# Performance work log

Hardware: AMD Instinct MI355X
Metric: run time of the kernel (lower is better)

Reference implementation:

```python
import jax, jax.numpy as jnp
import numpy as np

B = 262144
D = 128          # d_model
DFF = 4 * D      # 512, FFN expansion
T = 16           # num_tiles
TPC = 4          # tiles_per_cluster
NC = T // TPC    # 4 clusters
NOPS = 8         # len(OPCODES)
EMB = 32
FEAT = EMB + 17  # 49
TW, SW, DW = 0.01, 0.005, 0.01  # ternary / sparsity / diversity weights


def ternary_quant(W):
    # per-tile ternary quantization: threshold at 0.7 * mean|W|, scale = mean|W|
    s0 = jnp.mean(jnp.abs(W))
    return s0 * jnp.sign(W) * (jnp.abs(W) > 0.7 * s0).astype(W.dtype)


def setup_inputs() -> dict:
    key = jax.random.key(0)
    ks = jax.random.split(key, 16)
    inp = {
        'op_idx': jax.random.randint(ks[0], (B,), 0, NOPS),
        'a': jax.random.randint(ks[1], (B,), 0, 256),
        'b': jax.random.randint(ks[2], (B,), 0, 256),
        'c': jax.random.randint(ks[3], (B,), 0, 2),
        # parameters
        'op_embed': jax.random.normal(ks[4], (NOPS, EMB), jnp.float32),
        'W_in': jax.random.normal(ks[5], (FEAT, D), jnp.float32) / np.sqrt(FEAT),
        'b_in': jnp.zeros((D,), jnp.float32),
        'Wr': jax.random.normal(ks[6], (D, T), jnp.float32) / np.sqrt(D),
        'W1': jax.random.normal(ks[7], (T, D, DFF), jnp.float32) / np.sqrt(D),
        'W2': jax.random.normal(ks[8], (T, DFF, D), jnp.float32) / np.sqrt(DFF),
        'Wh1': jax.random.normal(ks[9], (D, 64), jnp.float32) / np.sqrt(D),
        'bh1': jnp.zeros((64,), jnp.float32),
        'Wh2': jax.random.normal(ks[10], (64, 8), jnp.float32) / np.sqrt(64),
        'bh2': jnp.zeros((8,), jnp.float32),
    }
    return inp


def reference(op_embed, W_in, b_in, Wr, W1, W2, Wh1, bh1, Wh2, bh2, op_idx, a, b, c):
    bits = lambda v: ((v[:, None] >> jnp.arange(8)) & 1).astype(jnp.float32)  # [B,8]
    emb = op_embed[op_idx]  # [B,32]
    x = jnp.concatenate([emb, bits(a), bits(b), c[:, None].astype(jnp.float32)], axis=1)  # [B,49]
    x = x @ W_in + b_in  # [B,D]

    # tile routing (top-1)
    logits = x @ Wr                      # [B,T]
    probs = jax.nn.softmax(logits, -1)
    idx = jnp.argmax(probs, -1)          # [B]
    gate = jnp.max(probs, -1)            # [B]

    # ternary-quantized per-tile FFN weights
    W1q = jax.vmap(ternary_quant)(W1)    # [T,D,DFF]
    W2q = jax.vmap(ternary_quant)(W2)    # [T,DFF,D]

    out = jnp.zeros_like(x)
    for t in range(T):  # fixed small tile set
        y = jax.nn.gelu(x @ W1q[t]) @ W2q[t]          # [B,D]
        out = out + jnp.where((idx == t)[:, None], y, 0.0)
    out = out * gate[:, None]

    # aux losses
    one_hot = jax.nn.one_hot(idx, T, dtype=x.dtype)
    frac = one_hot.mean(0)               # tokens per tile
    meanp = probs.mean(0)                # mean router prob per tile
    sparsity = T * jnp.sum(frac * meanp)              # load-balance (Switch-style)
    tern = jnp.mean(jnp.abs(W1 - W1q)) + jnp.mean(jnp.abs(W2 - W2q))
    cp = meanp.reshape(NC, TPC).sum(-1)               # cluster usage
    diversity = jnp.sum(cp * jnp.log(cp + 1e-9))      # negative entropy
    aux = TW * tern + SW * sparsity + DW * diversity

    h = jax.nn.relu(out @ Wh1 + bh1)
    result = jax.nn.sigmoid(h @ Wh2 + bh2)  # [B,8]
    return result, idx, aux
```

## Files before the change

kernel.cpp:

```cpp
#include <hip/hip_runtime.h>
#include <hip/hip_bf16.h>
#include <math.h>

typedef __attribute__((ext_vector_type(8))) short short8;
typedef __attribute__((ext_vector_type(4))) float floatx4;
typedef __attribute__((ext_vector_type(4))) unsigned int uintx4;

__device__ __forceinline__ unsigned short f2bf(float f) {
    unsigned int u = __float_as_uint(f);
    unsigned int r = (u + 0x7fffu + ((u >> 16) & 1u)) >> 16;
    return (unsigned short)r;
}

__device__ __forceinline__ unsigned int cvtpk(float a, float b) {
    unsigned int r;
    asm("v_cvt_pk_bf16_f32 %0, %1, %2" : "=v"(r) : "v"(a), "v"(b));
    return r;
}

__device__ __forceinline__ void permlane32_swap(unsigned int &a, unsigned int &b) {
    asm volatile("v_permlane32_swap_b32 %0, %1" : "+v"(a), "+v"(b));
}
__device__ __forceinline__ void permlane16_swap(unsigned int &a, unsigned int &b) {
    asm volatile("v_permlane16_swap_b32 %0, %1" : "+v"(a), "+v"(b));
}

__device__ __forceinline__ float gelu_f(float u) {
    float u2 = u * u;
    float p = __builtin_fmaf(u2, -0.102943242f, -2.302208184f);
    float z = p * u;
    float e;
    asm("v_exp_f32 %0, %1" : "=v"(e) : "v"(z));
    return u * __builtin_amdgcn_rcpf(1.0f + e);
}

__device__ __forceinline__ floatx4 mfma16(short8 a, short8 b, floatx4 c) {
    return __builtin_amdgcn_mfma_f32_16x16x32_bf16(a, b, c, 0, 0, 0);
}


__global__ __launch_bounds__(256) void k_prep1(
        const float* __restrict__ W1, const float* __restrict__ W2,
        float* __restrict__ partials,
        const float* __restrict__ op_embed, const float* __restrict__ W_in,
        const float* __restrict__ b_in,
        float* embW, float* Ta, float* Tb, float* Tc) {
    __shared__ float red[256];
    int bid = blockIdx.x;
    if (bid < 512) {
        bool isW1 = bid < 256;
        const float* W = (isW1 ? W1 : W2) + (long)(isW1 ? bid : bid - 256) * 4096;
        float s = 0.f;
        #pragma unroll
        for (int i = 0; i < 4; i++) {
            floatx4 v = *(const floatx4*)(W + i * 1024 + threadIdx.x * 4);
            s += fabsf(v[0]) + fabsf(v[1]) + fabsf(v[2]) + fabsf(v[3]);
        }
        red[threadIdx.x] = s; __syncthreads();
        for (int st = 128; st > 0; st >>= 1) {
            if (threadIdx.x < st) red[threadIdx.x] += red[threadIdx.x + st];
            __syncthreads();
        }
        if (threadIdx.x == 0) partials[bid] = red[0];
    } else {
        int i = (bid - 512) * 256 + threadIdx.x;
        if (i < 1024) {
            int op = i >> 7, j = i & 127;
            float s = b_in[j];
            #pragma unroll
            for (int k = 0; k < 32; k++) s += op_embed[op * 32 + k] * W_in[k * 128 + j];
            embW[i] = s;
        } else if (i < 1024 + 32768) {
            int r = i - 1024; int a = r >> 7, j = r & 127;
            float s = 0.f;
            #pragma unroll
            for (int bit = 0; bit < 8; bit++) if ((a >> bit) & 1) s += W_in[(32 + bit) * 128 + j];
            Ta[r] = s;
        } else if (i < 33792 + 32768) {
            int r = i - 33792; int b = r >> 7, j = r & 127;
            float s = 0.f;
            #pragma unroll
            for (int bit = 0; bit < 8; bit++) if ((b >> bit) & 1) s += W_in[(40 + bit) * 128 + j];
            Tb[r] = s;
        } else if (i < 66560 + 128) {
            int j = i - 66560; Tc[j] = W_in[48 * 128 + j];
        }
    }
}


__global__ __launch_bounds__(256) void k_prep2(
        const float* __restrict__ W1, const float* __restrict__ W2,
        const float* __restrict__ partials,
        unsigned short* __restrict__ W1qT, unsigned short* __restrict__ W2qT,
        float* ternsum,
        const float* __restrict__ embW, const float* __restrict__ Ta,
        const float* __restrict__ Tb, const float* __restrict__ Tc,
        const float* __restrict__ Wr,
        float* embWr, float* TaR, float* TbR, float* TcR) {
    __shared__ unsigned short Lq[4096];
    __shared__ float red[256];
    int blk = blockIdx.x;
    if (blk >= 512) {
        int i = (blk - 512) * 256 + threadIdx.x;
        int row = i >> 4, t = i & 15;
        const float* src; float* dst;
        if (row < 8)        { src = embW + row * 128;        dst = embWr + i; }
        else if (row < 264) { src = Ta + (row - 8) * 128;    dst = TaR + (row - 8) * 16 + t; }
        else if (row < 520) { src = Tb + (row - 264) * 128;  dst = TbR + (row - 264) * 16 + t; }
        else if (row == 520){ src = Tc;                      dst = TcR + t; }
        else return;
        float s = 0.f;
        for (int j = 0; j < 128; j++) s += src[j] * Wr[j * 16 + t];
        *dst = s;
        return;
    }
    bool isW1 = blk < 256;
    int rb = isW1 ? blk : blk - 256;
    int t = rb >> 4, slab = rb & 15;
    const float* part = partials + (isW1 ? 0 : 256) + t * 16;
    float ssum = 0.f;
    #pragma unroll
    for (int i = 0; i < 16; i++) ssum += part[i];
    float s = ssum * (1.0f / 65536.0f);
    float thr = 0.7f * s;
    unsigned int us = (unsigned int)f2bf(s);
    int tid = threadIdx.x;
    float dsum = 0.f;
    if (isW1) {
        int f0 = slab * 32;
        int d = tid >> 1, fh = (tid & 1) * 16;
        const float* src = W1 + (long)t * 65536 + d * 512 + f0 + fh;
        #pragma unroll
        for (int i = 0; i < 4; i++) {
            floatx4 w = *(const floatx4*)(src + i * 4);
            #pragma unroll
            for (int r = 0; r < 4; r++) {
                float wv = w[r];
                float aw = fabsf(wv);
                bool big = aw > thr;
                dsum += big ? fabsf(aw - s) : aw;
                unsigned int sign15 = (__float_as_uint(wv) >> 16) & 0x8000u;
                unsigned short q = big ? (unsigned short)(us | sign15) : (unsigned short)0;
                Lq[(fh + i * 4 + r) * 128 + d] = q;
            }
        }
    } else {
        int d0 = slab * 8;
        int f = tid * 2;
        const float* src = W2 + (long)t * 65536 + f * 128 + d0;
        #pragma unroll
        for (int rr = 0; rr < 2; rr++) {
            #pragma unroll
            for (int i = 0; i < 2; i++) {
                floatx4 w = *(const floatx4*)(src + rr * 128 + i * 4);
                #pragma unroll
                for (int r = 0; r < 4; r++) {
                    float wv = w[r];
                    float aw = fabsf(wv);
                    bool big = aw > thr;
                    dsum += big ? fabsf(aw - s) : aw;
                    unsigned int sign15 = (__float_as_uint(wv) >> 16) & 0x8000u;
                    unsigned short q = big ? (unsigned short)(us | sign15) : (unsigned short)0;
                    Lq[(i * 4 + r) * 512 + f + rr] = q;
                }
            }
        }
    }
    __syncthreads();
    unsigned short* dst = (isW1 ? W1qT : W2qT) + (long)t * 65536 + slab * 4096;
    const uintx4* Ls = (const uintx4*)Lq;
    uintx4* D4 = (uintx4*)dst;
    D4[tid] = Ls[tid];
    D4[tid + 256] = Ls[tid + 256];
    red[tid] = dsum; __syncthreads();
    for (int st2 = 128; st2 > 0; st2 >>= 1) {
        if (tid < st2) red[tid] += red[tid + st2];
        __syncthreads();
    }
    if (tid == 0) atomicAdd(ternsum, red[0]);
}


__global__ __launch_bounds__(256) void k_main3(
        const int* __restrict__ op_idx, const int* __restrict__ a_in,
        const int* __restrict__ b_in_i, const int* __restrict__ c_in,
        const float* __restrict__ embWr, const float* __restrict__ TaR,
        const float* __restrict__ TbR, const float* __restrict__ TcR,
        float* __restrict__ gate_out,
        float* psum, int* cnt, float* __restrict__ d_idx,
        const unsigned short* __restrict__ W2qT, const float* __restrict__ Wh1,
        unsigned short* __restrict__ W23qT) {
    __shared__ float sp[4][16];
    __shared__ int sc[4][16];
    __shared__ float wcol[128];

    if (blockIdx.x >= 1024) {
        int b2 = blockIdx.x - 1024;
        int t = b2 >> 6, h = b2 & 63;
        if (threadIdx.x < 128) wcol[threadIdx.x] = Wh1[threadIdx.x * 64 + h];
        __syncthreads();
        int k2 = threadIdx.x * 2;
        const unsigned short* w2 = W2qT + (long)t * 65536 + k2;
        float a0 = 0.f, a1 = 0.f;
        #pragma unroll 8
        for (int d = 0; d < 128; d++) {
            unsigned int u = *(const unsigned int*)(w2 + d * 512);
            float w = wcol[d];
            a0 += w * __uint_as_float(u << 16);
            a1 += w * __uint_as_float(u & 0xffff0000u);
        }
        *(unsigned int*)(W23qT + ((long)(t * 64 + h)) * 512 + k2) = cvtpk(a0, a1);
        return;
    }

    int gid = blockIdx.x * 256 + threadIdx.x;
    int lane = threadIdx.x & 63;
    int j = lane & 15;
    int grpbase = lane & 48;
    float psum_acc = 0.f; int cnt_acc = 0;

    #pragma unroll 1
    for (int it = 0; it < 16; it++) {
        int tok = it * 16384 + (gid >> 4);
        int op = op_idx[tok], a = a_in[tok], b = b_in_i[tok], c = c_in[tok];
        float cf = (float)c;

        float lg = embWr[op * 16 + j] + TaR[a * 16 + j] + TbR[b * 16 + j] + cf * TcR[j];
        float m = lg;
        m = fmaxf(m, __shfl_xor(m, 8, 16));
        m = fmaxf(m, __shfl_xor(m, 4, 16));
        m = fmaxf(m, __shfl_xor(m, 2, 16));
        m = fmaxf(m, __shfl_xor(m, 1, 16));
        float p = __expf(lg - m);
        float s = p;
        s += __shfl_xor(s, 8, 16);
        s += __shfl_xor(s, 4, 16);
        s += __shfl_xor(s, 2, 16);
        s += __shfl_xor(s, 1, 16);
        float g = __builtin_amdgcn_rcpf(s);
        unsigned long long ball = __ballot(lg == m);
        int bi = __ffsll((unsigned long long)((ball >> grpbase) & 0xffffULL)) - 1;
        psum_acc += p * g;
        cnt_acc += (j == bi) ? 1 : 0;
        if (j == 0) { gate_out[tok] = g; d_idx[tok] = (float)bi; }
    }

    psum_acc += __shfl_xor(psum_acc, 16);
    psum_acc += __shfl_xor(psum_acc, 32);
    cnt_acc += __shfl_xor(cnt_acc, 16);
    cnt_acc += __shfl_xor(cnt_acc, 32);
    int wv = threadIdx.x >> 6;
    if (lane < 16) { sp[wv][j] = psum_acc; sc[wv][j] = cnt_acc; }
    __syncthreads();
    if (threadIdx.x < 16) {
        int jj = threadIdx.x;
        atomicAdd(&psum[jj], sp[0][jj] + sp[1][jj] + sp[2][jj] + sp[3][jj]);
        atomicAdd(&cnt[jj], sc[0][jj] + sc[1][jj] + sc[2][jj] + sc[3][jj]);
    }
}


__global__ void k_scatter(const float* __restrict__ d_idx, const int* __restrict__ cnt,
                          int* fill, int* __restrict__ bucket) {
    __shared__ int lc[16], lbase[16];
    if (threadIdx.x < 16) lc[threadIdx.x] = 0;
    __syncthreads();
    int offs[16];
    {
        int off = 0;
        #pragma unroll
        for (int tt = 0; tt < 16; tt++) { offs[tt] = off; off += cnt[tt]; }
    }
    int tok = blockIdx.x * 256 + threadIdx.x;
    int t = (int)d_idx[tok];
    int lpos = atomicAdd(&lc[t], 1);
    __syncthreads();
    if (threadIdx.x < 16) lbase[threadIdx.x] = atomicAdd(&fill[threadIdx.x], lc[threadIdx.x]);
    __syncthreads();
    bucket[offs[t] + lbase[t] + lpos] = tok;
}


__global__ __launch_bounds__(256, 3) void k_ffn(
    const int* __restrict__ op_idx, const int* __restrict__ a_in,
    const int* __restrict__ b_in_i, const int* __restrict__ c_in,
    const float* __restrict__ embW, const float* __restrict__ Ta,
    const float* __restrict__ Tb, const float* __restrict__ Tc,
    const float* __restrict__ gate,
    const int* __restrict__ bucket, const int* __restrict__ cnt_g,
    const float* __restrict__ psum_g, const float* __restrict__ ternsum_g,
    const unsigned short* __restrict__ W1qT, const unsigned short* __restrict__ W23qT,
    const float* __restrict__ Wh2, const float* __restrict__ bh1,
    const float* __restrict__ bh2,
    float* __restrict__ result, float* __restrict__ d_aux) {

    extern __shared__ __align__(16) unsigned char smem[];
    unsigned short* Ax = (unsigned short*)smem;
    float* Red = (float*)(smem + 17408);
    int*   toks = (int*)(smem + 33792);
    float* gats = (float*)(smem + 34048);
    float* Wh2l = (float*)(smem + 34304);
    float* bh2l = (float*)(smem + 36352);
    float* bh1l = (float*)(smem + 36384);
    int*   opsl = (int*)(smem + 36640);
    int*   asl  = (int*)(smem + 36896);
    int*   bsl  = (int*)(smem + 37152);
    float* csl  = (float*)(smem + 37408);

    int bid = blockIdx.x;
    int t = -1, ci = 0, nt = 0, base = 0;
    {
        int coff = 0, off = 0;
        #pragma unroll 1
        for (int tt = 0; tt < 16; tt++) {
            int c = cnt_g[tt];
            int ch = (c + 63) >> 6;
            if (t < 0 && bid < coff + ch) { t = tt; ci = bid - coff; nt = c; base = off + ci * 64; }
            coff += ch; off += c;
        }
    }
    if (t < 0) return;
    int nvalid = nt - ci * 64; if (nvalid > 64) nvalid = 64;

    int tid = threadIdx.x;
    if (tid < 64) {
        int tk = (tid < nvalid) ? bucket[base + tid] : -1;
        toks[tid] = tk;
        int tks = (tk >= 0) ? tk : 0;
        gats[tid] = (tk >= 0) ? gate[tk] : 0.0f;
        opsl[tid] = op_idx[tks];
        asl[tid]  = a_in[tks];
        bsl[tid]  = b_in_i[tks];
        csl[tid]  = (float)c_in[tks];
    }
    Wh2l[tid] = Wh2[tid];
    Wh2l[tid + 256] = Wh2[tid + 256];
    if (tid < 8) bh2l[tid] = bh2[tid];
    else if (tid < 72) bh1l[tid - 8] = bh1[tid - 8];
    __syncthreads();

    #pragma unroll
    for (int it = 0; it < 4; it++) {
        int seg = it * 256 + tid; int r = seg >> 4, sg = seg & 15;
        int d0 = sg * 8;
        int op = opsl[r], a = asl[r], b = bsl[r];
        float cf = csl[r];
        const floatx4* Ev = (const floatx4*)(embW + op * 128 + d0);
        const floatx4* A4 = (const floatx4*)(Ta + a * 128 + d0);
        const floatx4* B4 = (const floatx4*)(Tb + b * 128 + d0);
        const floatx4* C4 = (const floatx4*)(Tc + d0);
        floatx4 v0 = Ev[0] + A4[0] + B4[0] + cf * C4[0];
        floatx4 v1 = Ev[1] + A4[1] + B4[1] + cf * C4[1];
        uintx4 o;
        o[0] = cvtpk(v0[0], v0[1]);
        o[1] = cvtpk(v0[2], v0[3]);
        o[2] = cvtpk(v1[0], v1[1]);
        o[3] = cvtpk(v1[2], v1[3]);
        *(uintx4*)(Ax + r * 136 + sg * 8) = o;
    }
    __syncthreads();

    int lane = tid & 63, dh = tid >> 6;
    int lane15 = lane & 15, lgrp = lane >> 4;

    floatx4 acc3[4][4];
    #pragma unroll
    for (int i = 0; i < 4; i++)
        #pragma unroll
        for (int j = 0; j < 4; j++) acc3[i][j] = (floatx4){0.f, 0.f, 0.f, 0.f};

    const unsigned short* w1p  = W1qT + (long)t * 65536 + (dh * 32 + lane15) * 128 + lgrp * 8;
    const unsigned short* w23p = W23qT + (long)t * 32768 + lane15 * 512 + dh * 32 + lgrp * 8;
    int ho0 = dh * 8192;
    int ho1 = ((dh + 1) & 3) * 8192;
    int ho2 = ((dh + 2) & 3) * 8192;
    int ho3 = ((dh + 3) & 3) * 8192;

    #pragma unroll
    for (int nc = 0; nc < 4; nc++) {
        const unsigned short* w1c = w1p + nc * 16384;
        const unsigned short* w23c = w23p + nc * 128;

        short8 a00 = *(const short8*)(w1c + 0 * 32);
        short8 a01 = *(const short8*)(w1c + 1 * 32);
        short8 a02 = *(const short8*)(w1c + 2 * 32);
        short8 a03 = *(const short8*)(w1c + 3 * 32);
        short8 a10 = *(const short8*)(w1c + 2048 + 0 * 32);
        short8 a11 = *(const short8*)(w1c + 2048 + 1 * 32);
        short8 a12 = *(const short8*)(w1c + 2048 + 2 * 32);
        short8 a13 = *(const short8*)(w1c + 2048 + 3 * 32);
        short8 af23_0 = *(const short8*)(w23c + ho0);
        short8 af23_1 = *(const short8*)(w23c + ho1);
        short8 af23_2 = *(const short8*)(w23c + ho2);
        short8 af23_3 = *(const short8*)(w23c + ho3);

        floatx4 acc1[2][4];
        #pragma unroll
        for (int i = 0; i < 2; i++)
            #pragma unroll
            for (int j = 0; j < 4; j++) acc1[i][j] = (floatx4){0.f, 0.f, 0.f, 0.f};

        #pragma unroll
        for (int mt = 0; mt < 4; mt++) {
            int mrow = (mt * 16 + lane15) * 136;
            short8 bf0 = *(const short8*)(Ax + mrow + 0 * 32 + lgrp * 8);
            short8 bf1 = *(const short8*)(Ax + mrow + 1 * 32 + lgrp * 8);
            short8 bf2 = *(const short8*)(Ax + mrow + 2 * 32 + lgrp * 8);
            short8 bf3 = *(const short8*)(Ax + mrow + 3 * 32 + lgrp * 8);
            acc1[0][mt] = mfma16(a00, bf0, acc1[0][mt]);
            acc1[1][mt] = mfma16(a10, bf0, acc1[1][mt]);
            acc1[0][mt] = mfma16(a01, bf1, acc1[0][mt]);
            acc1[1][mt] = mfma16(a11, bf1, acc1[1][mt]);
            acc1[0][mt] = mfma16(a02, bf2, acc1[0][mt]);
            acc1[1][mt] = mfma16(a12, bf2, acc1[1][mt]);
            acc1[0][mt] = mfma16(a03, bf3, acc1[0][mt]);
            acc1[1][mt] = mfma16(a13, bf3, acc1[1][mt]);
        }

        #pragma unroll
        for (int mt = 0; mt < 4; mt++) {
            floatx4 v0 = acc1[0][mt], v1 = acc1[1][mt];
            unsigned int X0 = cvtpk(gelu_f(v0[0]), gelu_f(v0[1]));
            unsigned int X1 = cvtpk(gelu_f(v0[2]), gelu_f(v0[3]));
            unsigned int Y0 = cvtpk(gelu_f(v1[0]), gelu_f(v1[1]));
            unsigned int Y1 = cvtpk(gelu_f(v1[2]), gelu_f(v1[3]));
            permlane32_swap(X0, Y0);
            permlane16_swap(X0, Y0);
            permlane32_swap(X1, Y1);
            permlane16_swap(X1, Y1);
            union { uintx4 u; short8 s; } bu;
            bu.u[0] = X0; bu.u[1] = X1; bu.u[2] = Y0; bu.u[3] = Y1;
            short8 bfrag = bu.s;
            acc3[0][mt] = mfma16(af23_0, bfrag, acc3[0][mt]);
            acc3[1][mt] = mfma16(af23_1, bfrag, acc3[1][mt]);
            acc3[2][mt] = mfma16(af23_2, bfrag, acc3[2][mt]);
            acc3[3][mt] = mfma16(af23_3, bfrag, acc3[3][mt]);
        }
    }

    floatx4 fin[4];
    #pragma unroll
    for (int mt = 0; mt < 4; mt++) fin[mt] = acc3[0][mt];
    float* myslot = Red + dh * 1024;
    int lofs = lane * 4;
    #pragma unroll
    for (int mt = 0; mt < 4; mt++)
        *(floatx4*)(myslot + mt * 256 + lofs) = acc3[1][mt];
    __syncthreads();
    {
        const float* ps = Red + ((dh + 3) & 3) * 1024;
        #pragma unroll
        for (int mt = 0; mt < 4; mt++)
            fin[mt] += *(const floatx4*)(ps + mt * 256 + lofs);
    }
    __syncthreads();
    #pragma unroll
    for (int mt = 0; mt < 4; mt++)
        *(floatx4*)(myslot + mt * 256 + lofs) = acc3[2][mt];
    __syncthreads();
    {
        const float* ps = Red + ((dh + 2) & 3) * 1024;
        #pragma unroll
        for (int mt = 0; mt < 4; mt++)
            fin[mt] += *(const floatx4*)(ps + mt * 256 + lofs);
    }
    __syncthreads();
    #pragma unroll
    for (int mt = 0; mt < 4; mt++)
        *(floatx4*)(myslot + mt * 256 + lofs) = acc3[3][mt];
    __syncthreads();
    {
        const float* ps = Red + ((dh + 1) & 3) * 1024;
        #pragma unroll
        for (int mt = 0; mt < 4; mt++)
            fin[mt] += *(const floatx4*)(ps + mt * 256 + lofs);
    }

    float* H = (float*)Ax;
    int hb = dh * 16 + lgrp * 4;
    floatx4 b4 = *(const floatx4*)(bh1l + hb);
    #pragma unroll
    for (int mt = 0; mt < 4; mt++) {
        int m = mt * 16 + lane15;
        float gm = gats[m];
        floatx4 v;
        v[0] = fmaxf(fin[mt][0] * gm + b4[0], 0.f);
        v[1] = fmaxf(fin[mt][1] * gm + b4[1], 0.f);
        v[2] = fmaxf(fin[mt][2] * gm + b4[2], 0.f);
        v[3] = fmaxf(fin[mt][3] * gm + b4[3], 0.f);
        *(floatx4*)(H + m * 68 + hb) = v;
    }
    __syncthreads();

    int mloc = tid >> 2, c0 = (tid & 3) * 2;
    int tk = toks[mloc];
    float z0 = bh2l[c0], z1 = bh2l[c0 + 1];
    const floatx4* Hr4 = (const floatx4*)(H + mloc * 68);
    #pragma unroll
    for (int h4 = 0; h4 < 16; h4++) {
        floatx4 hv = Hr4[h4];
        #pragma unroll
        for (int r = 0; r < 4; r++) {
            int h = h4 * 4 + r;
            z0 += hv[r] * Wh2l[h * 8 + c0];
            z1 += hv[r] * Wh2l[h * 8 + c0 + 1];
        }
    }
    if (tk >= 0) {
        float2 rr;
        rr.x = __builtin_amdgcn_rcpf(1.0f + __expf(-z0));
        rr.y = __builtin_amdgcn_rcpf(1.0f + __expf(-z1));
        *(float2*)(result + (long)tk * 8 + c0) = rr;
    }

    if (bid == 0 && tid == 0) {
        const float Bf = 262144.0f;
        float tern = ternsum_g[0] * (1.0f / 1048576.0f);
        float sp = 0.f; float cp[4] = {0.f, 0.f, 0.f, 0.f};
        for (int tt = 0; tt < 16; tt++) {
            float frac = (float)cnt_g[tt] / Bf, mp = psum_g[tt] / Bf;
            sp += frac * mp; cp[tt >> 2] += mp;
        }
        float dv = 0.f;
        for (int cc = 0; cc < 4; cc++) dv += cp[cc] * logf(cp[cc] + 1e-9f);
        d_aux[0] = 0.01f * tern + 0.005f * (16.0f * sp) + 0.01f * dv;
    }
}


extern "C" void kernel_launch(void* const* d_in, const int* in_sizes, int n_in,
                              void* d_out, int out_size, void* d_ws, size_t ws_size,
                              hipStream_t stream) {
    const int* op_idx = (const int*)d_in[0];
    const int* a_in   = (const int*)d_in[1];
    const int* b_in_i = (const int*)d_in[2];
    const int* c_in   = (const int*)d_in[3];
    const float* op_embed = (const float*)d_in[4];
    const float* W_in  = (const float*)d_in[5];
    const float* b_in  = (const float*)d_in[6];
    const float* Wr    = (const float*)d_in[7];
    const float* W1    = (const float*)d_in[8];
    const float* W2    = (const float*)d_in[9];
    const float* Wh1   = (const float*)d_in[10];
    const float* bh1   = (const float*)d_in[11];
    const float* Wh2   = (const float*)d_in[12];
    const float* bh2   = (const float*)d_in[13];

    const long B = in_sizes[0];
    float* result = (float*)d_out;
    float* d_idx  = (float*)d_out + B * 8;
    float* d_aux  = (float*)d_out + B * 9;

    unsigned char* ws = (unsigned char*)d_ws;
    unsigned short* W1qT  = (unsigned short*)(ws + 67108864);
    unsigned short* W2qT  = (unsigned short*)(ws + 69206016);
    unsigned short* W23qT = (unsigned short*)(ws + 71303168);
    float* gate  = (float*)(ws + 72351744);
    int*   bucket= (int*)  (ws + 73400320);
    float* Ta    = (float*)(ws + 74448896);
    float* Tb    = (float*)(ws + 74579968);
    float* embW  = (float*)(ws + 74711040);
    float* Tc    = (float*)(ws + 74715136);
    float* TaR   = (float*)(ws + 74715648);
    float* TbR   = (float*)(ws + 74732032);
    float* embWr = (float*)(ws + 74748416);
    float* TcR   = (float*)(ws + 74748928);
    float* partials = (float*)(ws + 74748992);
    unsigned char* acc = ws + 74751040;
    float* ternsum = (float*)(acc + 0);
    float* psum    = (float*)(acc + 64);
    int*   cnt     = (int*)(acc + 128);
    int*   fill    = (int*)(acc + 192);

    hipMemsetAsync(acc, 0, 256, stream);

    k_prep1<<<773, 256, 0, stream>>>(W1, W2, partials, op_embed, W_in, b_in,
                                     embW, Ta, Tb, Tc);
    k_prep2<<<545, 256, 0, stream>>>(W1, W2, partials, W1qT, W2qT, ternsum,
                                     embW, Ta, Tb, Tc, Wr, embWr, TaR, TbR, TcR);
    k_main3<<<2048, 256, 0, stream>>>(op_idx, a_in, b_in_i, c_in,
                                      embWr, TaR, TbR, TcR,
                                      gate, psum, cnt, d_idx,
                                      W2qT, Wh1, W23qT);
    k_scatter<<<(int)(B / 256), 256, 0, stream>>>(d_idx, cnt, fill, bucket);
    k_ffn<<<4112, 256, 37664, stream>>>(op_idx, a_in, b_in_i, c_in,
                                        embW, Ta, Tb, Tc,
                                        gate, bucket, cnt, psum, ternsum,
                                        W1qT, W23qT, Wh2, bh1, bh2, result, d_aux);
}
```

Baseline: 264.4 us.

## Fuse token scatter into router kernel using fixed-capacity per-tile buckets

Removes the separate k_scatter launch by having the router kernel record each token's tile and block-local position in shared memory, then reserve a global slice with one atomic per tile and write bucket entries directly. Buckets become fixed-capacity per-tile regions (BUCKET_CAP), so no prefix sum over counts is needed and the FFN kernel indexes tile*CAP. The FFN first GEMM is also restructured into a kk loop that loads W1 fragments per step instead of holding all eight at once, which lowers register pressure. The costs are a larger bucket workspace and extra shared atomics inside the router loop.

```diff
diff --git a/kernel.cpp b/kernel.cpp
--- a/kernel.cpp
+++ b/kernel.cpp
@@ -5,6 +5,8 @@
 typedef __attribute__((ext_vector_type(8))) short short8;
 typedef __attribute__((ext_vector_type(4))) float floatx4;
 typedef __attribute__((ext_vector_type(4))) unsigned int uintx4;
+
+#define BUCKET_CAP 262144
 
 __device__ __forceinline__ unsigned short f2bf(float f) {
     unsigned int u = __float_as_uint(f);
@@ -188,12 +190,16 @@
         const float* __restrict__ embWr, const float* __restrict__ TaR,
         const float* __restrict__ TbR, const float* __restrict__ TcR,
         float* __restrict__ gate_out,
-        float* psum, int* cnt, float* __restrict__ d_idx,
+        float* psum, int* cnt, int* fill, int* __restrict__ bucket,
+        float* __restrict__ d_idx,
         const unsigned short* __restrict__ W2qT, const float* __restrict__ Wh1,
         unsigned short* __restrict__ W23qT) {
     __shared__ float sp[4][16];
     __shared__ int sc[4][16];
     __shared__ float wcol[128];
+    __shared__ int lc[16], lbase[16];
+    __shared__ unsigned char blE[256];
+    __shared__ unsigned char lpE[256];
 
     if (blockIdx.x >= 1024) {
         int b2 = blockIdx.x - 1024;
@@ -214,10 +220,15 @@
         return;
     }
 
-    int gid = blockIdx.x * 256 + threadIdx.x;
-    int lane = threadIdx.x & 63;
+    int tid = threadIdx.x;
+    if (tid < 16) lc[tid] = 0;
+    __syncthreads();
+
+    int gid = blockIdx.x * 256 + tid;
+    int lane = tid & 63;
     int j = lane & 15;
     int grpbase = lane & 48;
+    int tl = tid >> 4;
     float psum_acc = 0.f; int cnt_acc = 0;
 
     #pragma unroll 1
@@ -243,6 +254,12 @@
         int bi = __ffsll((unsigned long long)((ball >> grpbase) & 0xffffULL)) - 1;
         psum_acc += p * g;
         cnt_acc += (j == bi) ? 1 : 0;
+        if (j == bi) {
+            int lpos = atomicAdd(&lc[bi], 1);
+            int e = it * 16 + tl;
+            blE[e] = (unsigned char)bi;
+            lpE[e] = (unsigned char)lpos;
+        }
         if (j == 0) { gate_out[tok] = g; d_idx[tok] = (float)bi; }
     }
 
@@ -250,35 +267,21 @@
     psum_acc += __shfl_xor(psum_acc, 32);
     cnt_acc += __shfl_xor(cnt_acc, 16);
     cnt_acc += __shfl_xor(cnt_acc, 32);
-    int wv = threadIdx.x >> 6;
+    int wv = tid >> 6;
     if (lane < 16) { sp[wv][j] = psum_acc; sc[wv][j] = cnt_acc; }
     __syncthreads();
-    if (threadIdx.x < 16) {
-        int jj = threadIdx.x;
-        atomicAdd(&psum[jj], sp[0][jj] + sp[1][jj] + sp[2][jj] + sp[3][jj]);
-        atomicAdd(&cnt[jj], sc[0][jj] + sc[1][jj] + sc[2][jj] + sc[3][jj]);
-    }
-}
-
-
-__global__ void k_scatter(const float* __restrict__ d_idx, const int* __restrict__ cnt,
-                          int* fill, int* __restrict__ bucket) {
-    __shared__ int lc[16], lbase[16];
-    if (threadIdx.x < 16) lc[threadIdx.x] = 0;
-    __syncthreads();
-    int offs[16];
+    if (tid < 16) {
+        atomicAdd(&psum[tid], sp[0][tid] + sp[1][tid] + sp[2][tid] + sp[3][tid]);
+        atomicAdd(&cnt[tid], sc[0][tid] + sc[1][tid] + sc[2][tid] + sc[3][tid]);
+        lbase[tid] = atomicAdd(&fill[tid], lc[tid]);
+    }
+    __syncthreads();
     {
-        int off = 0;
-        #pragma unroll
-        for (int tt = 0; tt < 16; tt++) { offs[tt] = off; off += cnt[tt]; }
-    }
-    int tok = blockIdx.x * 256 + threadIdx.x;
-    int t = (int)d_idx[tok];
-    int lpos = atomicAdd(&lc[t], 1);
-    __syncthreads();
-    if (threadIdx.x < 16) lbase[threadIdx.x] = atomicAdd(&fill[threadIdx.x], lc[threadIdx.x]);
-    __syncthreads();
-    bucket[offs[t] + lbase[t] + lpos] = tok;
+        int e = tid;
+        int bi = (int)blE[e];
+        int tok = (e >> 4) * 16384 + blockIdx.x * 16 + (e & 15);
+        bucket[bi * BUCKET_CAP + lbase[bi] + (int)lpE[e]] = tok;
+    }
 }
 
 
@@ -311,13 +314,16 @@
     int bid = blockIdx.x;
     int t = -1, ci = 0, nt = 0, base = 0;
     {
-        int coff = 0, off = 0;
+        int coff = 0;
         #pragma unroll 1
         for (int tt = 0; tt < 16; tt++) {
             int c = cnt_g[tt];
             int ch = (c + 63) >> 6;
-            if (t < 0 && bid < coff + ch) { t = tt; ci = bid - coff; nt = c; base = off + ci * 64; }
-            coff += ch; off += c;
+            if (t < 0 && bid < coff + ch) {
+                t = tt; ci = bid - coff; nt = c;
+                base = tt * BUCKET_CAP + ci * 64;
+            }
+            coff += ch;
         }
     }
     if (t < 0) return;
@@ -377,46 +383,32 @@
     int ho2 = ((dh + 2) & 3) * 8192;
     int ho3 = ((dh + 3) & 3) * 8192;
 
-    #pragma unroll
     for (int nc = 0; nc < 4; nc++) {
+        floatx4 acc1[2][4];
+        #pragma unroll
+        for (int i = 0; i < 2; i++)
+            #pragma unroll
+            for (int j = 0; j < 4; j++) acc1[i][j] = (floatx4){0.f, 0.f, 0.f, 0.f};
+
         const unsigned short* w1c = w1p + nc * 16384;
+        #pragma unroll
+        for (int kk = 0; kk < 4; kk++) {
+            short8 af0 = *(const short8*)(w1c + kk * 32);
+            short8 af1 = *(const short8*)(w1c + 2048 + kk * 32);
+            int ko = kk * 32 + lgrp * 8;
+            #pragma unroll
+            for (int mt = 0; mt < 4; mt++) {
+                short8 bf = *(const short8*)(Ax + (mt * 16 + lane15) * 136 + ko);
+                acc1[0][mt] = mfma16(af0, bf, acc1[0][mt]);
+                acc1[1][mt] = mfma16(af1, bf, acc1[1][mt]);
+            }
+        }
+
         const unsigned short* w23c = w23p + nc * 128;
-
-        short8 a00 = *(const short8*)(w1c + 0 * 32);
-        short8 a01 = *(const short8*)(w1c + 1 * 32);
-        short8 a02 = *(const short8*)(w1c + 2 * 32);
-        short8 a03 = *(const short8*)(w1c + 3 * 32);
-        short8 a10 = *(const short8*)(w1c + 2048 + 0 * 32);
-        short8 a11 = *(const short8*)(w1c + 2048 + 1 * 32);
-        short8 a12 = *(const short8*)(w1c + 2048 + 2 * 32);
-        short8 a13 = *(const short8*)(w1c + 2048 + 3 * 32);
         short8 af23_0 = *(const short8*)(w23c + ho0);
         short8 af23_1 = *(const short8*)(w23c + ho1);
         short8 af23_2 = *(const short8*)(w23c + ho2);
         short8 af23_3 = *(const short8*)(w23c + ho3);
-
-        floatx4 acc1[2][4];
-        #pragma unroll
-        for (int i = 0; i < 2; i++)
-            #pragma unroll
-            for (int j = 0; j < 4; j++) acc1[i][j] = (floatx4){0.f, 0.f, 0.f, 0.f};
-
-        #pragma unroll
-        for (int mt = 0; mt < 4; mt++) {
-            int mrow = (mt * 16 + lane15) * 136;
-            short8 bf0 = *(const short8*)(Ax + mrow + 0 * 32 + lgrp * 8);
-            short8 bf1 = *(const short8*)(Ax + mrow + 1 * 32 + lgrp * 8);
-            short8 bf2 = *(const short8*)(Ax + mrow + 2 * 32 + lgrp * 8);
-            short8 bf3 = *(const short8*)(Ax + mrow + 3 * 32 + lgrp * 8);
-            acc1[0][mt] = mfma16(a00, bf0, acc1[0][mt]);
-            acc1[1][mt] = mfma16(a10, bf0, acc1[1][mt]);
-            acc1[0][mt] = mfma16(a01, bf1, acc1[0][mt]);
-            acc1[1][mt] = mfma16(a11, bf1, acc1[1][mt]);
-            acc1[0][mt] = mfma16(a02, bf2, acc1[0][mt]);
-            acc1[1][mt] = mfma16(a12, bf2, acc1[1][mt]);
-            acc1[0][mt] = mfma16(a03, bf3, acc1[0][mt]);
-            acc1[1][mt] = mfma16(a13, bf3, acc1[1][mt]);
-        }
 
         #pragma unroll
         for (int mt = 0; mt < 4; mt++) {
@@ -553,11 +545,11 @@
     float* d_aux  = (float*)d_out + B * 9;
 
     unsigned char* ws = (unsigned char*)d_ws;
+    int*   bucket= (int*)(ws + 0);
     unsigned short* W1qT  = (unsigned short*)(ws + 67108864);
     unsigned short* W2qT  = (unsigned short*)(ws + 69206016);
     unsigned short* W23qT = (unsigned short*)(ws + 71303168);
     float* gate  = (float*)(ws + 72351744);
-    int*   bucket= (int*)  (ws + 73400320);
     float* Ta    = (float*)(ws + 74448896);
     float* Tb    = (float*)(ws + 74579968);
     float* embW  = (float*)(ws + 74711040);
@@ -581,9 +573,8 @@
                                      embW, Ta, Tb, Tc, Wr, embWr, TaR, TbR, TcR);
     k_main3<<<2048, 256, 0, stream>>>(op_idx, a_in, b_in_i, c_in,
                                       embWr, TaR, TbR, TcR,
-                                      gate, psum, cnt, d_idx,
+                                      gate, psum, cnt, fill, bucket, d_idx,
                                       W2qT, Wh1, W23qT);
-    k_scatter<<<(int)(B / 256), 256, 0, stream>>>(d_idx, cnt, fill, bucket);
     k_ffn<<<4112, 256, 37664, stream>>>(op_idx, a_in, b_in_i, c_in,
                                         embW, Ta, Tb, Tc,
                                         gate, bucket, cnt, psum, ternsum,
```

Measured after the change: 252.6 us. -4.5%, faster.
